# Kernel optimization log

Hardware: AMD Instinct MI355X
Metric: run time of the kernel (lower is better)

Reference implementation:

```python
import jax, jax.numpy as jnp
import numpy as np

B, L, N, F, H, HOR = 32, 12, 1024, 2, 128, 12


def setup_inputs() -> dict:
    key = jax.random.key(0)
    ks = jax.random.split(key, 9)
    x = jax.random.normal(ks[0], (B, L, N, F), dtype=jnp.float32)
    # A_phys: sparse-ish binary physical adjacency, then normalize_adj: add self-loops, row-normalize
    A_phys = (jax.random.uniform(ks[1], (N, N)) < 0.05).astype(jnp.float32)
    A = A_phys + jnp.eye(N, dtype=jnp.float32)
    A = A / (A.sum(axis=1, keepdims=True) + 1e-6)
    # GraphGRUCell params (single layer): lin_x: F -> 3H, lin_h: H -> 3H
    sx = 1.0 / np.sqrt(F)
    sh = 1.0 / np.sqrt(H)
    W_x = jax.random.uniform(ks[2], (F, 3 * H), minval=-sx, maxval=sx)
    b_x = jax.random.uniform(ks[3], (3 * H,), minval=-sx, maxval=sx)
    W_h = jax.random.uniform(ks[4], (H, 3 * H), minval=-sh, maxval=sh)
    b_h = jax.random.uniform(ks[5], (3 * H,), minval=-sh, maxval=sh)
    # head: H -> horizon
    W_head = jax.random.uniform(ks[6], (H, HOR), minval=-sh, maxval=sh)
    b_head = jax.random.uniform(ks[7], (HOR,), minval=-sh, maxval=sh)
    return {"x": x, "A": A, "W_x": W_x, "b_x": b_x, "W_h": W_h, "b_h": b_h,
            "W_head": W_head, "b_head": b_head}


def reference(x, A, W_x, b_x, W_h, b_h, W_head, b_head):
    Bv, Lv, Nv, Fv = x.shape
    Hv = W_h.shape[0]

    def step(h, xt):
        # graph aggregation of hidden state: [N,N] x [B,N,H] -> [B,N,H]
        Ah = jnp.einsum('ij,bjh->bih', A, h)
        x_gates = xt @ W_x + b_x          # [B,N,3H]
        h_gates = Ah @ W_h + b_h          # [B,N,3H]
        z_x, r_x, n_x = jnp.split(x_gates, 3, axis=-1)
        z_h, r_h, n_h = jnp.split(h_gates, 3, axis=-1)
        z = jax.nn.sigmoid(z_x + z_h)
        r = jax.nn.sigmoid(r_x + r_h)
        n = jnp.tanh(n_x + r * n_h)
        h_new = (1.0 - z) * n + z * h
        return h_new, None

    h0 = jnp.zeros((Bv, Nv, Hv), dtype=x.dtype)
    xs = jnp.moveaxis(x, 1, 0)  # [L,B,N,F]
    h, _ = jax.lax.scan(step, h0, xs)
    y = (h @ W_head + b_head).transpose(0, 2, 1)  # [B, horizon, N]
    return y
```

## Files before the change

kernel.cpp:

```cpp
#include <hip/hip_runtime.h>
#include <hip/hip_bf16.h>

#define BB 32
#define LL 12
#define NN 1024
#define FF 2
#define HH 128
#define HORN 12
#define G3 384

typedef unsigned short u16;
typedef unsigned int u32;
typedef unsigned long long u64;
typedef __attribute__((ext_vector_type(8))) short short8;
typedef __attribute__((ext_vector_type(4))) float f32x4;

__device__ __forceinline__ u16 to_bf16(float f) {
    return __builtin_bit_cast(u16, __float2bfloat16(f));
}
__device__ __forceinline__ float bf_to_f(u32 bits) {
    return __builtin_bit_cast(float, bits << 16);
}

__global__ void prep_abf(const float* __restrict__ A, u16* __restrict__ Abf) {
    int t = blockIdx.x * blockDim.x + threadIdx.x;
    float4 v = ((const float4*)A)[t];
    ushort4 o;
    o.x = to_bf16(v.x); o.y = to_bf16(v.y); o.z = to_bf16(v.z); o.w = to_bf16(v.w);
    ((ushort4*)Abf)[t] = o;
}

__global__ void prep_whT(const float* __restrict__ W_h, u16* __restrict__ whT) {
    int t = blockIdx.x * blockDim.x + threadIdx.x;
    if (t >= HH * G3) return;
    int c = t / HH, k = t % HH;
    whT[c * HH + k] = to_bf16(W_h[k * G3 + c]);
}

__global__ __launch_bounds__(512, 4) void gru_step(
    const u16* __restrict__ Abf, const u16* __restrict__ hT_old,
    u16* __restrict__ hT_new, const u16* __restrict__ whT,
    const float* __restrict__ x, const float* __restrict__ W_x,
    const float* __restrict__ b_x, const float* __restrict__ b_h, int t) {
    __shared__ __align__(16) char smem[49152];

    int bid = blockIdx.x;
    int swz = (bid & 7) * 64 + (bid >> 3);
    int b = swz >> 4;
    int i0 = (swz & 15) * 64;
    int tid = threadIdx.x;
    int w = tid >> 6, lane = tid & 63;
    int lcol = lane & 15, kgrp = lane >> 4;
    int wm = w >> 2, wn = w & 3;

    int s_r = tid >> 3;
    int s_c = (tid & 7) * 8;
    const u16* a_src = Abf + (size_t)(i0 + s_r) * 1024 + s_c;
    const u16* b_src = hT_old + (size_t)b * 131072 + (size_t)s_r * 1024 + s_c;
    u32 swb = (u32)((s_c * 2) ^ ((s_r & 7) << 4));
    u32 a_wo = (u32)(s_r * 128) + swb;
    u32 b_wo = 8192u + (u32)(s_r * 128) + swb;

    int ar = wm * 32 + lcol;
    u32 a_base = (u32)(ar * 128), a_swz = (u32)((ar & 7) << 4);
    int bn = wn * 32 + lcol;
    u32 b_base = 8192u + (u32)(bn * 128), b_swz = (u32)((bn & 7) << 4);

    f32x4 acc[2][2] = {{{0.f,0.f,0.f,0.f},{0.f,0.f,0.f,0.f}},
                       {{0.f,0.f,0.f,0.f},{0.f,0.f,0.f,0.f}}};

    uint4 ra = *(const uint4*)a_src;
    uint4 rb0 = *(const uint4*)b_src;
    uint4 rb1 = *(const uint4*)(b_src + 65536);
    *(uint4*)(smem + a_wo) = ra;
    *(uint4*)(smem + b_wo) = rb0;
    *(uint4*)(smem + b_wo + 8192) = rb1;

    for (int c = 0; c < 16; ++c) {
        __syncthreads();
        uint4 na, nb0, nb1;
        bool pf = (c < 15);
        if (pf) {
            int o = (c + 1) * 64;
            na  = *(const uint4*)(a_src + o);
            nb0 = *(const uint4*)(b_src + o);
            nb1 = *(const uint4*)(b_src + o + 65536);
        }
        u32 sb = (u32)((c & 1) * 24576);
#pragma unroll
        for (int ks = 0; ks < 2; ++ks) {
            u32 kb = (u32)(ks * 64 + kgrp * 16);
            short8 af0 = *(const short8*)(smem + sb + a_base + (kb ^ a_swz));
            short8 af1 = *(const short8*)(smem + sb + a_base + 2048 + (kb ^ a_swz));
            short8 bf0 = *(const short8*)(smem + sb + b_base + (kb ^ b_swz));
            short8 bf1 = *(const short8*)(smem + sb + b_base + 2048 + (kb ^ b_swz));
            acc[0][0] = __builtin_amdgcn_mfma_f32_16x16x32_bf16(af0, bf0, acc[0][0], 0, 0, 0);
            acc[0][1] = __builtin_amdgcn_mfma_f32_16x16x32_bf16(af0, bf1, acc[0][1], 0, 0, 0);
            acc[1][0] = __builtin_amdgcn_mfma_f32_16x16x32_bf16(af1, bf0, acc[1][0], 0, 0, 0);
            acc[1][1] = __builtin_amdgcn_mfma_f32_16x16x32_bf16(af1, bf1, acc[1][1], 0, 0, 0);
        }
        if (pf) {
            u32 db = (u32)(((c + 1) & 1) * 24576);
            *(uint4*)(smem + db + a_wo) = na;
            *(uint4*)(smem + db + b_wo) = nb0;
            *(uint4*)(smem + db + b_wo + 8192) = nb1;
        }
    }

#pragma unroll
    for (int mt = 0; mt < 2; ++mt) {
#pragma unroll
        for (int nt = 0; nt < 2; ++nt) {
#pragma unroll
            for (int ri = 0; ri < 4; ++ri) {
                int row = wm * 32 + mt * 16 + kgrp * 4 + ri;
                int col = wn * 32 + nt * 16 + lcol;
                *(u16*)(smem + row * 256 + ((2 * col) ^ ((row & 7) << 4))) = to_bf16(acc[mt][nt][ri]);
            }
        }
    }
    __syncthreads();

    int hh = w * 16 + lcol;
    short8 bw[3][4];
#pragma unroll
    for (int g = 0; g < 3; ++g)
#pragma unroll
        for (int ks = 0; ks < 4; ++ks)
            bw[g][ks] = *(const short8*)(whT + (size_t)(g * 128 + hh) * 128 + ks * 32 + kgrp * 8);

    f32x4 acc2[4][3];
#pragma unroll
    for (int rt = 0; rt < 4; ++rt)
#pragma unroll
        for (int g = 0; g < 3; ++g) acc2[rt][g] = (f32x4){0.f, 0.f, 0.f, 0.f};

#pragma unroll
    for (int rt = 0; rt < 4; ++rt) {
        int r2 = rt * 16 + lcol;
        u32 ab2 = (u32)(r2 * 256), as2 = (u32)((r2 & 7) << 4);
#pragma unroll
        for (int ks = 0; ks < 4; ++ks) {
            short8 a2 = *(const short8*)(smem + ab2 + ((ks * 64 + kgrp * 16) ^ as2));
            acc2[rt][0] = __builtin_amdgcn_mfma_f32_16x16x32_bf16(a2, bw[0][ks], acc2[rt][0], 0, 0, 0);
            acc2[rt][1] = __builtin_amdgcn_mfma_f32_16x16x32_bf16(a2, bw[1][ks], acc2[rt][1], 0, 0, 0);
            acc2[rt][2] = __builtin_amdgcn_mfma_f32_16x16x32_bf16(a2, bw[2][ks], acc2[rt][2], 0, 0, 0);
        }
    }

    float bxz = b_x[hh], bxr = b_x[128 + hh], bxn = b_x[256 + hh];
    float bhz = b_h[hh], bhr = b_h[128 + hh], bhn = b_h[256 + hh];
    float wx0z = W_x[hh], wx0r = W_x[128 + hh], wx0n = W_x[256 + hh];
    float wx1z = W_x[G3 + hh], wx1r = W_x[G3 + 128 + hh], wx1n = W_x[G3 + 256 + hh];
    const u16* hrow = hT_old + (size_t)b * 131072 + (size_t)hh * 1024 + i0;
#pragma unroll
    for (int rt = 0; rt < 4; ++rt) {
        u64 h4 = *(const u64*)(hrow + rt * 16 + kgrp * 4);
#pragma unroll
        for (int ri = 0; ri < 4; ++ri) {
            int rl = rt * 16 + kgrp * 4 + ri;
            int i = i0 + rl;
            const float* xp = x + ((size_t)(b * LL + t) * NN + i) * FF;
            float x0 = xp[0], x1 = xp[1];
            float zin = acc2[rt][0][ri] + bhz + fmaf(x0, wx0z, fmaf(x1, wx1z, bxz));
            float rin = acc2[rt][1][ri] + bhr + fmaf(x0, wx0r, fmaf(x1, wx1r, bxr));
            float z = 1.f / (1.f + __expf(-zin));
            float rg = 1.f / (1.f + __expf(-rin));
            float nin = fmaf(rg, acc2[rt][2][ri] + bhn, fmaf(x0, wx0n, fmaf(x1, wx1n, bxn)));
            nin = fmaxf(nin, -40.f);
            float e = __expf(-2.f * nin);
            float n = (1.f - e) / (1.f + e);
            float hold = bf_to_f((u32)((h4 >> (16 * ri)) & 0xffffu));
            float hv = fmaf(z, hold - n, n);
            *(u16*)(smem + 16384 + hh * 128 + ((2 * rl) ^ ((hh & 7) << 4))) = to_bf16(hv);
        }
    }
    __syncthreads();
#pragma unroll
    for (int c2 = 0; c2 < 2; ++c2) {
        int o = tid * 32 + c2 * 16;
        int nrow = o >> 7, cbb = o & 127;
        uint4 v = *(const uint4*)(smem + 16384 + nrow * 128 + (cbb ^ ((nrow & 7) << 4)));
        *(uint4*)((char*)(hT_new + ((size_t)b * 128 + nrow) * 1024 + i0) + cbb) = v;
    }
}

__global__ __launch_bounds__(256) void head_kernel(
    const u16* __restrict__ hT, const float* __restrict__ W_head,
    const float* __restrict__ b_head, float* __restrict__ out) {
    __shared__ float wl[HH * HORN];
    __shared__ float bl[HORN];
    int tid = threadIdx.x;
    for (int ix = tid; ix < HH * HORN; ix += 256) wl[ix] = W_head[ix];
    if (tid < HORN) bl[tid] = b_head[tid];
    __syncthreads();
    int blk = blockIdx.x;
    int b = blk >> 2;
    int i = (blk & 3) * 256 + tid;
    const u16* hp = hT + (size_t)b * 131072 + i;
    float acc[HORN];
#pragma unroll
    for (int hor = 0; hor < HORN; ++hor) acc[hor] = bl[hor];
    for (int hh = 0; hh < HH; ++hh) {
        float hv = bf_to_f((u32)hp[hh * 1024]);
#pragma unroll
        for (int hor = 0; hor < HORN; ++hor)
            acc[hor] = fmaf(hv, wl[hh * HORN + hor], acc[hor]);
    }
#pragma unroll
    for (int hor = 0; hor < HORN; ++hor)
        out[((size_t)b * HORN + hor) * NN + i] = acc[hor];
}

extern "C" void kernel_launch(void* const* d_in, const int* in_sizes, int n_in,
                              void* d_out, int out_size, void* d_ws, size_t ws_size,
                              hipStream_t stream) {
    const float* x = (const float*)d_in[0];
    const float* A = (const float*)d_in[1];
    const float* W_x = (const float*)d_in[2];
    const float* b_x = (const float*)d_in[3];
    const float* W_h = (const float*)d_in[4];
    const float* b_h = (const float*)d_in[5];
    const float* W_head = (const float*)d_in[6];
    const float* b_head = (const float*)d_in[7];
    float* out = (float*)d_out;
    char* ws = (char*)d_ws;

    u16* hT0 = (u16*)(ws + 0);
    u16* hT1 = (u16*)(ws + 8388608);
    u16* Abf = (u16*)(ws + 16777216);
    u16* whT = (u16*)(ws + 18874368);

    hipMemsetAsync(hT0, 0, 8388608, stream);
    prep_abf<<<1024, 256, 0, stream>>>(A, Abf);
    prep_whT<<<(HH * G3 + 255) / 256, 256, 0, stream>>>(W_h, whT);

    u16* hTo = hT0; u16* hTn = hT1;
    for (int t = 0; t < LL; ++t) {
        gru_step<<<512, 512, 0, stream>>>(Abf, hTo, hTn, whT, x, W_x, b_x, b_h, t);
        u16* tmp = hTo; hTo = hTn; hTn = tmp;
    }
    head_kernel<<<BB * 4, 256, 0, stream>>>(hTo, W_head, b_head, out);
}
```

Baseline: 343.8 us.

## Use direct global-to-LDS loads, larger per-wave tiles, and skip the zero-state first step

The A·h loop now copies tiles straight from global memory into LDS with global_load_lds, instead of staging them through registers. Source addresses are pre-swizzled so the LDS layout stays conflict-free. Blocks shrink from 512 to 256 threads, and each wave computes a 32x64 tile and two hidden sub-slices, which gives more reuse per wave. A FIRST template variant skips the aggregation GEMM and the h_old load at t=0 because h is zero there, and that removes the memset. The trade-offs are more registers per thread, fewer waves for hiding latency, and a 64KB LDS footprint.

```diff
diff --git a/kernel.cpp b/kernel.cpp
--- a/kernel.cpp
+++ b/kernel.cpp
@@ -4,7 +4,6 @@
 #define BB 32
 #define LL 12
 #define NN 1024
-#define FF 2
 #define HH 128
 #define HORN 12
 #define G3 384
@@ -20,6 +19,10 @@
 }
 __device__ __forceinline__ float bf_to_f(u32 bits) {
     return __builtin_bit_cast(float, bits << 16);
+}
+__device__ __forceinline__ void gl16(const u16* g, char* l) {
+    __builtin_amdgcn_global_load_lds((const __attribute__((address_space(1))) u32*)g,
+                                     (__attribute__((address_space(3))) u32*)l, 16, 0, 0);
 }
 
 __global__ void prep_abf(const float* __restrict__ A, u16* __restrict__ Abf) {
@@ -37,12 +40,13 @@
     whT[c * HH + k] = to_bf16(W_h[k * G3 + c]);
 }
 
-__global__ __launch_bounds__(512, 4) void gru_step(
+template <bool FIRST>
+__global__ __launch_bounds__(256, 2) void gru_step(
     const u16* __restrict__ Abf, const u16* __restrict__ hT_old,
     u16* __restrict__ hT_new, const u16* __restrict__ whT,
     const float* __restrict__ x, const float* __restrict__ W_x,
     const float* __restrict__ b_x, const float* __restrict__ b_h, int t) {
-    __shared__ __align__(16) char smem[49152];
+    __shared__ __align__(16) char smem[65536];
 
     int bid = blockIdx.x;
     int swz = (bid & 7) * 64 + (bid >> 3);
@@ -51,137 +55,150 @@
     int tid = threadIdx.x;
     int w = tid >> 6, lane = tid & 63;
     int lcol = lane & 15, kgrp = lane >> 4;
-    int wm = w >> 2, wn = w & 3;
-
-    int s_r = tid >> 3;
-    int s_c = (tid & 7) * 8;
-    const u16* a_src = Abf + (size_t)(i0 + s_r) * 1024 + s_c;
-    const u16* b_src = hT_old + (size_t)b * 131072 + (size_t)s_r * 1024 + s_c;
-    u32 swb = (u32)((s_c * 2) ^ ((s_r & 7) << 4));
-    u32 a_wo = (u32)(s_r * 128) + swb;
-    u32 b_wo = 8192u + (u32)(s_r * 128) + swb;
-
-    int ar = wm * 32 + lcol;
-    u32 a_base = (u32)(ar * 128), a_swz = (u32)((ar & 7) << 4);
-    int bn = wn * 32 + lcol;
-    u32 b_base = 8192u + (u32)(bn * 128), b_swz = (u32)((bn & 7) << 4);
-
-    f32x4 acc[2][2] = {{{0.f,0.f,0.f,0.f},{0.f,0.f,0.f,0.f}},
-                       {{0.f,0.f,0.f,0.f},{0.f,0.f,0.f,0.f}}};
-
-    uint4 ra = *(const uint4*)a_src;
-    uint4 rb0 = *(const uint4*)b_src;
-    uint4 rb1 = *(const uint4*)(b_src + 65536);
-    *(uint4*)(smem + a_wo) = ra;
-    *(uint4*)(smem + b_wo) = rb0;
-    *(uint4*)(smem + b_wo + 8192) = rb1;
-
-    for (int c = 0; c < 16; ++c) {
+    int wm = w >> 1, wn = w & 1;
+    u32 swzl = (u32)((lcol & 7) << 4);
+
+    u32 a_b = (u32)((wm * 32 + lcol) * 128);
+    u32 b_b = (u32)(8192 + (wn * 64 + lcol) * 128);
+
+    f32x4 acc[2][4];
+#pragma unroll
+    for (int m = 0; m < 2; ++m)
+#pragma unroll
+        for (int n = 0; n < 4; ++n) acc[m][n] = (f32x4){0.f, 0.f, 0.f, 0.f};
+
+    if (!FIRST) {
+        int lr3 = lane >> 3, lc8 = lane & 7;
+        const u16* ag[2]; u32 al[2];
+        const u16* bg[4]; u32 bl[4];
+#pragma unroll
+        for (int q = 0; q < 2; ++q) {
+            int r = w * 16 + q * 8 + lr3;
+            ag[q] = Abf + (size_t)(i0 + r) * 1024 + (lc8 ^ (r & 7)) * 8;
+            al[q] = (u32)(w * 2048 + q * 1024);
+        }
+#pragma unroll
+        for (int q = 0; q < 4; ++q) {
+            int r = w * 32 + q * 8 + lr3;
+            bg[q] = hT_old + (size_t)b * 131072 + (size_t)r * 1024 + (lc8 ^ (r & 7)) * 8;
+            bl[q] = (u32)(8192 + w * 4096 + q * 1024);
+        }
+
+#pragma unroll
+        for (int q = 0; q < 2; ++q) gl16(ag[q], smem + al[q]);
+#pragma unroll
+        for (int q = 0; q < 4; ++q) gl16(bg[q], smem + bl[q]);
         __syncthreads();
-        uint4 na, nb0, nb1;
-        bool pf = (c < 15);
-        if (pf) {
-            int o = (c + 1) * 64;
-            na  = *(const uint4*)(a_src + o);
-            nb0 = *(const uint4*)(b_src + o);
-            nb1 = *(const uint4*)(b_src + o + 65536);
-        }
-        u32 sb = (u32)((c & 1) * 24576);
-#pragma unroll
-        for (int ks = 0; ks < 2; ++ks) {
-            u32 kb = (u32)(ks * 64 + kgrp * 16);
-            short8 af0 = *(const short8*)(smem + sb + a_base + (kb ^ a_swz));
-            short8 af1 = *(const short8*)(smem + sb + a_base + 2048 + (kb ^ a_swz));
-            short8 bf0 = *(const short8*)(smem + sb + b_base + (kb ^ b_swz));
-            short8 bf1 = *(const short8*)(smem + sb + b_base + 2048 + (kb ^ b_swz));
-            acc[0][0] = __builtin_amdgcn_mfma_f32_16x16x32_bf16(af0, bf0, acc[0][0], 0, 0, 0);
-            acc[0][1] = __builtin_amdgcn_mfma_f32_16x16x32_bf16(af0, bf1, acc[0][1], 0, 0, 0);
-            acc[1][0] = __builtin_amdgcn_mfma_f32_16x16x32_bf16(af1, bf0, acc[1][0], 0, 0, 0);
-            acc[1][1] = __builtin_amdgcn_mfma_f32_16x16x32_bf16(af1, bf1, acc[1][1], 0, 0, 0);
-        }
-        if (pf) {
-            u32 db = (u32)(((c + 1) & 1) * 24576);
-            *(uint4*)(smem + db + a_wo) = na;
-            *(uint4*)(smem + db + b_wo) = nb0;
-            *(uint4*)(smem + db + b_wo + 8192) = nb1;
-        }
-    }
-
-#pragma unroll
-    for (int mt = 0; mt < 2; ++mt) {
-#pragma unroll
-        for (int nt = 0; nt < 2; ++nt) {
+
+        for (int c = 0; c < 16; ++c) {
+            u32 sb = (u32)((c & 1) * 24576);
+            if (c < 15) {
+                int o = (c + 1) * 64;
+                u32 db = (u32)(((c + 1) & 1) * 24576);
+#pragma unroll
+                for (int q = 0; q < 2; ++q) gl16(ag[q] + o, smem + db + al[q]);
+#pragma unroll
+                for (int q = 0; q < 4; ++q) gl16(bg[q] + o, smem + db + bl[q]);
+            }
+#pragma unroll
+            for (int ks = 0; ks < 2; ++ks) {
+                u32 kb = ((u32)(ks * 64 + kgrp * 16)) ^ swzl;
+                short8 a0 = *(const short8*)(smem + sb + a_b + kb);
+                short8 a1 = *(const short8*)(smem + sb + a_b + 2048 + kb);
+                short8 b0 = *(const short8*)(smem + sb + b_b + kb);
+                short8 b1 = *(const short8*)(smem + sb + b_b + 2048 + kb);
+                short8 b2 = *(const short8*)(smem + sb + b_b + 4096 + kb);
+                short8 b3 = *(const short8*)(smem + sb + b_b + 6144 + kb);
+                acc[0][0] = __builtin_amdgcn_mfma_f32_16x16x32_bf16(a0, b0, acc[0][0], 0, 0, 0);
+                acc[0][1] = __builtin_amdgcn_mfma_f32_16x16x32_bf16(a0, b1, acc[0][1], 0, 0, 0);
+                acc[0][2] = __builtin_amdgcn_mfma_f32_16x16x32_bf16(a0, b2, acc[0][2], 0, 0, 0);
+                acc[0][3] = __builtin_amdgcn_mfma_f32_16x16x32_bf16(a0, b3, acc[0][3], 0, 0, 0);
+                acc[1][0] = __builtin_amdgcn_mfma_f32_16x16x32_bf16(a1, b0, acc[1][0], 0, 0, 0);
+                acc[1][1] = __builtin_amdgcn_mfma_f32_16x16x32_bf16(a1, b1, acc[1][1], 0, 0, 0);
+                acc[1][2] = __builtin_amdgcn_mfma_f32_16x16x32_bf16(a1, b2, acc[1][2], 0, 0, 0);
+                acc[1][3] = __builtin_amdgcn_mfma_f32_16x16x32_bf16(a1, b3, acc[1][3], 0, 0, 0);
+            }
+            __syncthreads();
+        }
+    }
+
+#pragma unroll
+    for (int m = 0; m < 2; ++m)
+#pragma unroll
+        for (int n = 0; n < 4; ++n)
 #pragma unroll
             for (int ri = 0; ri < 4; ++ri) {
-                int row = wm * 32 + mt * 16 + kgrp * 4 + ri;
-                int col = wn * 32 + nt * 16 + lcol;
-                *(u16*)(smem + row * 256 + ((2 * col) ^ ((row & 7) << 4))) = to_bf16(acc[mt][nt][ri]);
-            }
-        }
-    }
+                int row = wm * 32 + m * 16 + kgrp * 4 + ri;
+                int col = wn * 64 + n * 16 + lcol;
+                *(u16*)(smem + 49152 + row * 256 + (((u32)(2 * col)) ^ ((u32)(row & 7) << 4))) =
+                    to_bf16(acc[m][n][ri]);
+            }
     __syncthreads();
 
-    int hh = w * 16 + lcol;
-    short8 bw[3][4];
-#pragma unroll
-    for (int g = 0; g < 3; ++g)
-#pragma unroll
-        for (int ks = 0; ks < 4; ++ks)
-            bw[g][ks] = *(const short8*)(whT + (size_t)(g * 128 + hh) * 128 + ks * 32 + kgrp * 8);
-
-    f32x4 acc2[4][3];
-#pragma unroll
-    for (int rt = 0; rt < 4; ++rt)
-#pragma unroll
-        for (int g = 0; g < 3; ++g) acc2[rt][g] = (f32x4){0.f, 0.f, 0.f, 0.f};
-
-#pragma unroll
-    for (int rt = 0; rt < 4; ++rt) {
-        int r2 = rt * 16 + lcol;
-        u32 ab2 = (u32)(r2 * 256), as2 = (u32)((r2 & 7) << 4);
-#pragma unroll
-        for (int ks = 0; ks < 4; ++ks) {
-            short8 a2 = *(const short8*)(smem + ab2 + ((ks * 64 + kgrp * 16) ^ as2));
-            acc2[rt][0] = __builtin_amdgcn_mfma_f32_16x16x32_bf16(a2, bw[0][ks], acc2[rt][0], 0, 0, 0);
-            acc2[rt][1] = __builtin_amdgcn_mfma_f32_16x16x32_bf16(a2, bw[1][ks], acc2[rt][1], 0, 0, 0);
-            acc2[rt][2] = __builtin_amdgcn_mfma_f32_16x16x32_bf16(a2, bw[2][ks], acc2[rt][2], 0, 0, 0);
-        }
-    }
-
-    float bxz = b_x[hh], bxr = b_x[128 + hh], bxn = b_x[256 + hh];
-    float bhz = b_h[hh], bhr = b_h[128 + hh], bhn = b_h[256 + hh];
-    float wx0z = W_x[hh], wx0r = W_x[128 + hh], wx0n = W_x[256 + hh];
-    float wx1z = W_x[G3 + hh], wx1r = W_x[G3 + 128 + hh], wx1n = W_x[G3 + 256 + hh];
-    const u16* hrow = hT_old + (size_t)b * 131072 + (size_t)hh * 1024 + i0;
-#pragma unroll
-    for (int rt = 0; rt < 4; ++rt) {
-        u64 h4 = *(const u64*)(hrow + rt * 16 + kgrp * 4);
-#pragma unroll
-        for (int ri = 0; ri < 4; ++ri) {
-            int rl = rt * 16 + kgrp * 4 + ri;
-            int i = i0 + rl;
-            const float* xp = x + ((size_t)(b * LL + t) * NN + i) * FF;
-            float x0 = xp[0], x1 = xp[1];
-            float zin = acc2[rt][0][ri] + bhz + fmaf(x0, wx0z, fmaf(x1, wx1z, bxz));
-            float rin = acc2[rt][1][ri] + bhr + fmaf(x0, wx0r, fmaf(x1, wx1r, bxr));
-            float z = 1.f / (1.f + __expf(-zin));
-            float rg = 1.f / (1.f + __expf(-rin));
-            float nin = fmaf(rg, acc2[rt][2][ri] + bhn, fmaf(x0, wx0n, fmaf(x1, wx1n, bxn)));
-            nin = fmaxf(nin, -40.f);
-            float e = __expf(-2.f * nin);
-            float n = (1.f - e) / (1.f + e);
-            float hold = bf_to_f((u32)((h4 >> (16 * ri)) & 0xffffu));
-            float hv = fmaf(z, hold - n, n);
-            *(u16*)(smem + 16384 + hh * 128 + ((2 * rl) ^ ((hh & 7) << 4))) = to_bf16(hv);
+#pragma unroll
+    for (int sub = 0; sub < 2; ++sub) {
+        int hh = w * 32 + sub * 16 + lcol;
+        short8 bw[3][4];
+#pragma unroll
+        for (int g = 0; g < 3; ++g)
+#pragma unroll
+            for (int ks = 0; ks < 4; ++ks)
+                bw[g][ks] = *(const short8*)(whT + (size_t)(g * 128 + hh) * 128 + ks * 32 + kgrp * 8);
+
+        f32x4 acc2[4][3];
+#pragma unroll
+        for (int rt = 0; rt < 4; ++rt)
+#pragma unroll
+            for (int g = 0; g < 3; ++g) acc2[rt][g] = (f32x4){0.f, 0.f, 0.f, 0.f};
+
+#pragma unroll
+        for (int rt = 0; rt < 4; ++rt) {
+            u32 ab2 = (u32)(49152 + (rt * 16 + lcol) * 256);
+#pragma unroll
+            for (int ks = 0; ks < 4; ++ks) {
+                short8 a2 = *(const short8*)(smem + ab2 + (((u32)(ks * 64 + kgrp * 16)) ^ swzl));
+                acc2[rt][0] = __builtin_amdgcn_mfma_f32_16x16x32_bf16(a2, bw[0][ks], acc2[rt][0], 0, 0, 0);
+                acc2[rt][1] = __builtin_amdgcn_mfma_f32_16x16x32_bf16(a2, bw[1][ks], acc2[rt][1], 0, 0, 0);
+                acc2[rt][2] = __builtin_amdgcn_mfma_f32_16x16x32_bf16(a2, bw[2][ks], acc2[rt][2], 0, 0, 0);
+            }
+        }
+
+        float bxz = b_x[hh], bxr = b_x[128 + hh], bxn = b_x[256 + hh];
+        float bhz = b_h[hh], bhr = b_h[128 + hh], bhn = b_h[256 + hh];
+        float wx0z = W_x[hh], wx0r = W_x[128 + hh], wx0n = W_x[256 + hh];
+        float wx1z = W_x[G3 + hh], wx1r = W_x[G3 + 128 + hh], wx1n = W_x[G3 + 256 + hh];
+        const u16* hrow = hT_old + (size_t)b * 131072 + (size_t)hh * 1024 + i0;
+#pragma unroll
+        for (int rt = 0; rt < 4; ++rt) {
+            u64 h4 = 0;
+            if (!FIRST) h4 = *(const u64*)(hrow + rt * 16 + kgrp * 4);
+#pragma unroll
+            for (int ri = 0; ri < 4; ++ri) {
+                int rl = rt * 16 + kgrp * 4 + ri;
+                int i = i0 + rl;
+                const float* xp = x + ((size_t)(b * LL + t) * NN + i) * 2;
+                float x0 = xp[0], x1 = xp[1];
+                float zin = acc2[rt][0][ri] + bhz + fmaf(x0, wx0z, fmaf(x1, wx1z, bxz));
+                float rin = acc2[rt][1][ri] + bhr + fmaf(x0, wx0r, fmaf(x1, wx1r, bxr));
+                float z = 1.f / (1.f + __expf(-zin));
+                float rg = 1.f / (1.f + __expf(-rin));
+                float nin = fmaf(rg, acc2[rt][2][ri] + bhn, fmaf(x0, wx0n, fmaf(x1, wx1n, bxn)));
+                nin = fmaxf(nin, -40.f);
+                float e = __expf(-2.f * nin);
+                float n = (1.f - e) / (1.f + e);
+                float hold = bf_to_f((u32)((h4 >> (16 * ri)) & 0xffffu));
+                float hv = fmaf(z, hold - n, n);
+                *(u16*)(smem + hh * 128 + (((u32)(2 * rl)) ^ ((u32)(hh & 7) << 4))) = to_bf16(hv);
+            }
         }
     }
     __syncthreads();
 #pragma unroll
-    for (int c2 = 0; c2 < 2; ++c2) {
-        int o = tid * 32 + c2 * 16;
-        int nrow = o >> 7, cbb = o & 127;
-        uint4 v = *(const uint4*)(smem + 16384 + nrow * 128 + (cbb ^ ((nrow & 7) << 4)));
-        *(uint4*)((char*)(hT_new + ((size_t)b * 128 + nrow) * 1024 + i0) + cbb) = v;
+    for (int c2 = 0; c2 < 4; ++c2) {
+        int o = c2 * 4096 + tid * 16;
+        int nr = o >> 7, cb = o & 127;
+        uint4 v = *(const uint4*)(smem + nr * 128 + (((u32)cb) ^ ((u32)(nr & 7) << 4)));
+        *(uint4*)((char*)(hT_new + (size_t)b * 131072 + (size_t)nr * 1024 + i0) + cb) = v;
     }
 }
 
@@ -231,13 +248,13 @@
     u16* Abf = (u16*)(ws + 16777216);
     u16* whT = (u16*)(ws + 18874368);
 
-    hipMemsetAsync(hT0, 0, 8388608, stream);
     prep_abf<<<1024, 256, 0, stream>>>(A, Abf);
     prep_whT<<<(HH * G3 + 255) / 256, 256, 0, stream>>>(W_h, whT);
 
+    gru_step<true><<<512, 256, 0, stream>>>(Abf, hT1, hT0, whT, x, W_x, b_x, b_h, 0);
     u16* hTo = hT0; u16* hTn = hT1;
-    for (int t = 0; t < LL; ++t) {
-        gru_step<<<512, 512, 0, stream>>>(Abf, hTo, hTn, whT, x, W_x, b_x, b_h, t);
+    for (int t = 1; t < LL; ++t) {
+        gru_step<false><<<512, 256, 0, stream>>>(Abf, hTo, hTn, whT, x, W_x, b_x, b_h, t);
         u16* tmp = hTo; hTo = hTn; hTn = tmp;
     }
     head_kernel<<<BB * 4, 256, 0, stream>>>(hTo, W_head, b_head, out);
```

Measured after the change: 324.6 us. -5.6%, faster.
